# Performance work log

Measured on AMD Instinct MI355X. Metric: run time of the kernel, lower is better.

## Reference

```python
import jax, jax.numpy as jnp
import numpy as np


def setup_inputs() -> dict:
    key = jax.random.key(0)
    k1, k2 = jax.random.split(key)
    b, n, d = 8, 8192, 512
    x = jax.random.normal(k1, (b, n, d), dtype=jnp.float32)
    # t holds 2n-2 Toeplitz coefficients per channel; forward only uses the first n rows.
    t = jax.random.normal(k2, (2 * n - 2, d), dtype=jnp.float32)
    return {"x": x, "t": t}


def reference(x, t):
    """Per-channel causal cumulative weighted sum (the math of the naive quadruple loop):
        o[i, u, j] = sum_{v=0}^{u} t[v, j] * x[i, v, j]
    x: (b, n, d), t: (2n-2, d) -> o: (b, n, d)
    """
    n = x.shape[1]
    # broadcast t over batch, fuse elementwise product, then inclusive cumsum along seq
    return jnp.cumsum(x * t[None, :n, :], axis=1)
```

## Files before the change

kernel.cpp:

```cpp
#include <hip/hip_runtime.h>


typedef float f4 __attribute__((ext_vector_type(4)));

#define D  512
#define DV (D / 4)

__global__ __launch_bounds__(DV) void k_chunksum(
    const float* __restrict__ x, const float* __restrict__ t,
    float* __restrict__ S, int b, int n, int L) {
  const int c  = blockIdx.x / b;
  const int i  = blockIdx.x % b;
  const int jv = threadIdx.x;
  const size_t row0 = (size_t)c * L;
  const f4* xp = (const f4*)x + ((size_t)i * n + row0) * DV + jv;
  const f4* tp = (const f4*)t + row0 * DV + jv;
  f4 acc = {0.f, 0.f, 0.f, 0.f};
#pragma unroll 8
  for (int v = 0; v < L; ++v) {
    acc += xp[(size_t)v * DV] * tp[(size_t)v * DV];
  }
  ((f4*)S)[((size_t)c * b + i) * DV + jv] = acc;
}

__global__ __launch_bounds__(256) void k_scan(float* __restrict__ S, int b, int C) {
  const int tid = blockIdx.x * 256 + threadIdx.x;
  if (tid >= b * DV) return;
  const int i  = tid / DV;
  const int jv = tid % DV;
  f4 run = {0.f, 0.f, 0.f, 0.f};
  for (int c = 0; c < C; ++c) {
    f4* p = (f4*)S + ((size_t)c * b + i) * DV + jv;
    f4 s = *p;
    *p = run;
    run += s;
  }
}

__global__ __launch_bounds__(DV) void k_out(
    const float* __restrict__ x, const float* __restrict__ t,
    const float* __restrict__ S, float* __restrict__ o, int b, int n, int L) {
  const int c  = blockIdx.x / b;
  const int i  = blockIdx.x % b;
  const int jv = threadIdx.x;
  const size_t row0  = (size_t)c * L;
  const size_t xbase = ((size_t)i * n + row0) * DV + jv;
  const f4* xp = (const f4*)x + xbase;
  const f4* tp = (const f4*)t + row0 * DV + jv;
  f4*       op = (f4*)o + xbase;
  f4 acc = ((const f4*)S)[((size_t)c * b + i) * DV + jv];
#pragma unroll 4
  for (int v = 0; v < L; ++v) {
    acc += xp[(size_t)v * DV] * tp[(size_t)v * DV];
    op[(size_t)v * DV] = acc;
  }
}

__global__ __launch_bounds__(256) void k_naive(
    const float* __restrict__ x, const float* __restrict__ t,
    float* __restrict__ o, int b, int n) {
  const int tid = blockIdx.x * 256 + threadIdx.x;
  if (tid >= b * DV) return;
  const int i  = tid / DV;
  const int jv = tid % DV;
  const f4* xp = (const f4*)x + (size_t)i * n * DV + jv;
  const f4* tp = (const f4*)t + jv;
  f4*       op = (f4*)o + (size_t)i * n * DV + jv;
  f4 acc = {0.f, 0.f, 0.f, 0.f};
  for (int v = 0; v < n; ++v) {
    acc += xp[(size_t)v * DV] * tp[(size_t)v * DV];
    op[(size_t)v * DV] = acc;
  }
}

extern "C" void kernel_launch(void* const* d_in, const int* in_sizes, int n_in,
                              void* d_out, int out_size, void* d_ws, size_t ws_size,
                              hipStream_t stream) {
  const float* x = (const float*)d_in[0];
  const float* t = (const float*)d_in[1];
  float*       o = (float*)d_out;

  const long long t_elems = in_sizes[1];
  const int n = (int)((t_elems / D + 2) / 2);
  const int b = (int)((long long)in_sizes[0] / ((long long)n * D));

  const int C = 128;
  const size_t need = (size_t)C * b * D * sizeof(float);

  if (n % C == 0 && ws_size >= need) {
    const int L = n / C;
    float* S = (float*)d_ws;
    hipLaunchKernelGGL(k_chunksum, dim3(C * b), dim3(DV), 0, stream, x, t, S, b, n, L);
    const int scan_threads = b * DV;
    hipLaunchKernelGGL(k_scan, dim3((scan_threads + 255) / 256), dim3(256), 0, stream, S, b, C);
    hipLaunchKernelGGL(k_out, dim3(C * b), dim3(DV), 0, stream, x, t, S, o, b, n, L);
  } else {
    const int threads = b * DV;
    hipLaunchKernelGGL(k_naive, dim3((threads + 255) / 256), dim3(256), 0, stream, x, t, o, b, n);
  }
}
```

Baseline: 330.6 us.

## Drop scan kernel, fold chunk-prefix into output kernel, split chunksum rows

The serial k_scan launch is removed. Each k_out block now sums the chunk totals of all preceding chunks itself before running its local cumulative pass. k_chunksum uses four times as many threads, each covering a quarter of the chunk rows, and combines the partials through shared memory. This removes one launch and the serialized 128-step scan. The cost is redundant reads of S in k_out, up to 127 loads per thread in later chunks.

```diff
diff --git a/kernel.cpp b/kernel.cpp
--- a/kernel.cpp
+++ b/kernel.cpp
@@ -5,35 +5,31 @@
 
 #define D  512
 #define DV (D / 4)
+#define C  128
+#define RS 4
 
-__global__ __launch_bounds__(DV) void k_chunksum(
+__global__ __launch_bounds__(DV * RS) void k_chunksum(
     const float* __restrict__ x, const float* __restrict__ t,
     float* __restrict__ S, int b, int n, int L) {
   const int c  = blockIdx.x / b;
   const int i  = blockIdx.x % b;
-  const int jv = threadIdx.x;
-  const size_t row0 = (size_t)c * L;
+  const int jv = threadIdx.x & (DV - 1);
+  const int h  = threadIdx.x >> 7;
+  const int rows = L / RS;
+  const size_t row0 = (size_t)c * L + (size_t)h * rows;
   const f4* xp = (const f4*)x + ((size_t)i * n + row0) * DV + jv;
   const f4* tp = (const f4*)t + row0 * DV + jv;
   f4 acc = {0.f, 0.f, 0.f, 0.f};
 #pragma unroll 8
-  for (int v = 0; v < L; ++v) {
+  for (int v = 0; v < rows; ++v) {
     acc += xp[(size_t)v * DV] * tp[(size_t)v * DV];
   }
-  ((f4*)S)[((size_t)c * b + i) * DV + jv] = acc;
-}
-
-__global__ __launch_bounds__(256) void k_scan(float* __restrict__ S, int b, int C) {
-  const int tid = blockIdx.x * 256 + threadIdx.x;
-  if (tid >= b * DV) return;
-  const int i  = tid / DV;
-  const int jv = tid % DV;
-  f4 run = {0.f, 0.f, 0.f, 0.f};
-  for (int c = 0; c < C; ++c) {
-    f4* p = (f4*)S + ((size_t)c * b + i) * DV + jv;
-    f4 s = *p;
-    *p = run;
-    run += s;
+  __shared__ f4 red[RS][DV];
+  red[h][jv] = acc;
+  __syncthreads();
+  if (h == 0) {
+    f4 s = red[0][jv] + red[1][jv] + red[2][jv] + red[3][jv];
+    ((f4*)S)[((size_t)c * b + i) * DV + jv] = s;
   }
 }
 
@@ -43,12 +39,20 @@
   const int c  = blockIdx.x / b;
   const int i  = blockIdx.x % b;
   const int jv = threadIdx.x;
+
+  f4 acc = {0.f, 0.f, 0.f, 0.f};
+  const f4* Sp = (const f4*)S + (size_t)i * DV + jv;
+  const size_t cstride = (size_t)b * DV;
+#pragma unroll 8
+  for (int cp = 0; cp < c; ++cp) {
+    acc += Sp[(size_t)cp * cstride];
+  }
+
   const size_t row0  = (size_t)c * L;
   const size_t xbase = ((size_t)i * n + row0) * DV + jv;
   const f4* xp = (const f4*)x + xbase;
   const f4* tp = (const f4*)t + row0 * DV + jv;
   f4*       op = (f4*)o + xbase;
-  f4 acc = ((const f4*)S)[((size_t)c * b + i) * DV + jv];
 #pragma unroll 4
   for (int v = 0; v < L; ++v) {
     acc += xp[(size_t)v * DV] * tp[(size_t)v * DV];
@@ -84,18 +88,18 @@
   const int n = (int)((t_elems / D + 2) / 2);
   const int b = (int)((long long)in_sizes[0] / ((long long)n * D));
 
-  const int C = 128;
   const size_t need = (size_t)C * b * D * sizeof(float);
 
-  if (n % C == 0 && ws_size >= need) {
+  if (n % C == 0 && (n / C) % RS == 0 && ws_size >= need) {
     const int L = n / C;
     float* S = (float*)d_ws;
-    hipLaunchKernelGGL(k_chunksum, dim3(C * b), dim3(DV), 0, stream, x, t, S, b, n, L);
-    const int scan_threads = b * DV;
-    hipLaunchKernelGGL(k_scan, dim3((scan_threads + 255) / 256), dim3(256), 0, stream, S, b, C);
-    hipLaunchKernelGGL(k_out, dim3(C * b), dim3(DV), 0, stream, x, t, S, o, b, n, L);
+    hipLaunchKernelGGL(k_chunksum, dim3(C * b), dim3(DV * RS), 0, stream,
+                       x, t, S, b, n, L);
+    hipLaunchKernelGGL(k_out, dim3(C * b), dim3(DV), 0, stream,
+                       x, t, S, o, b, n, L);
   } else {
     const int threads = b * DV;
-    hipLaunchKernelGGL(k_naive, dim3((threads + 255) / 256), dim3(256), 0, stream, x, t, o, b, n);
+    hipLaunchKernelGGL(k_naive, dim3((threads + 255) / 256), dim3(256), 0, stream,
+                       x, t, o, b, n);
   }
 }
```

After: 300.8 us. -9.0%, faster.
